# Optimization experiments

Measured on AMD Instinct MI355X. Metric: run time of the kernel, lower is better.

Reference implementation:

```python
import jax, jax.numpy as jnp
import numpy as np

NB_OBJECTS = 3
DIM_BODY = 10
DIM_OBJECT = 15
DIM_OBJ_FEAT = NB_OBJECTS + DIM_OBJECT  # 18
DIM_PHI_IN = 54
HID = 256
DIM_PHI_OUT = 256
DIM_RHO_OUT = 1
B = 65536

# (o1, o2) object pair and (j, k) predicate indices, as in the torch code
PAIRS = [((0, 1), (3, 5)), ((0, 2), (4, 7)), ((1, 2), (6, 8))]


def setup_inputs() -> dict:
    key = jax.random.key(0)
    ks = jax.random.split(key, 24)
    inp = {
        "obs": jax.random.normal(ks[0], (B, 55), dtype=jnp.float32),
        "ag": jax.random.uniform(ks[1], (B, 9), dtype=jnp.float32),
        "g": jax.random.uniform(ks[2], (B, 9), dtype=jnp.float32),
        "anchor_g": jax.random.uniform(ks[3], (B, 9), dtype=jnp.float32),
        "act": jax.random.normal(ks[4], (B, 4), dtype=jnp.float32),
    }
    s = 0.05
    # PhiCriticDeepSet: two independent 2-layer MLPs (streams 1 and 2)
    inp["w1"] = jax.random.normal(ks[5], (DIM_PHI_IN, HID), dtype=jnp.float32) * s
    inp["b1"] = jnp.zeros((HID,), dtype=jnp.float32)
    inp["w2"] = jax.random.normal(ks[6], (HID, DIM_PHI_OUT), dtype=jnp.float32) * s
    inp["b2"] = jnp.zeros((DIM_PHI_OUT,), dtype=jnp.float32)
    inp["w3"] = jax.random.normal(ks[7], (DIM_PHI_IN, HID), dtype=jnp.float32) * s
    inp["b3"] = jnp.zeros((HID,), dtype=jnp.float32)
    inp["w4"] = jax.random.normal(ks[8], (HID, DIM_PHI_OUT), dtype=jnp.float32) * s
    inp["b4"] = jnp.zeros((DIM_PHI_OUT,), dtype=jnp.float32)
    # RhoCriticDeepSet: two independent 2-layer heads
    inp["w5"] = jax.random.normal(ks[9], (DIM_PHI_OUT, HID), dtype=jnp.float32) * s
    inp["b5"] = jnp.zeros((HID,), dtype=jnp.float32)
    inp["w6"] = jax.random.normal(ks[10], (HID, DIM_RHO_OUT), dtype=jnp.float32) * s
    inp["b6"] = jnp.zeros((DIM_RHO_OUT,), dtype=jnp.float32)
    inp["w7"] = jax.random.normal(ks[11], (DIM_PHI_OUT, HID), dtype=jnp.float32) * s
    inp["b7"] = jnp.zeros((HID,), dtype=jnp.float32)
    inp["w8"] = jax.random.normal(ks[12], (HID, DIM_RHO_OUT), dtype=jnp.float32) * s
    inp["b8"] = jnp.zeros((DIM_RHO_OUT,), dtype=jnp.float32)
    return inp


def _build_pair_inputs(obs, ag, g, act, anchor_g):
    """combinations_trick branch: data-dependent gather of goal bits and object pairs."""
    bs = obs.shape[0]
    obs_body = obs[:, :DIM_BODY]
    eye = jnp.eye(NB_OBJECTS, dtype=obs.dtype)
    # obs_objects: [3, B, 18] = one-hot(3) ++ object state(15)
    obs_objects = jnp.stack([
        jnp.concatenate([jnp.broadcast_to(eye[i], (bs, NB_OBJECTS)),
                         obs[:, DIM_BODY + DIM_OBJECT * i: DIM_BODY + DIM_OBJECT * (i + 1)]],
                        axis=1)
        for i in range(NB_OBJECTS)], axis=0)
    bidx = jnp.arange(bs)
    inputs = []
    for i, ((o1, o2), (j, k)) in enumerate(PAIRS):
        # selector = anchor_g @ [e_j, e_k] difference = anchor_g[:, j] - anchor_g[:, k]
        sel = (anchor_g[:, j] - anchor_g[:, k]) >= 0  # [B] bool
        # idxs_bits[i] = [i, j] where sel else [i, k]
        bit2 = jnp.where(sel, j, k)  # [B] int
        ag_pair = jnp.stack([ag[:, i], ag[bidx, bit2]], axis=1)  # [B, 2]
        g_pair = jnp.stack([g[:, i], g[bidx, bit2]], axis=1)     # [B, 2]
        # idxs_objects[i] = [o1, o2] where sel else [o2, o1]
        oi = jnp.where(sel, o1, o2)  # [B]
        oj = jnp.where(sel, o2, o1)
        obj_first = obs_objects[oi, bidx]   # [B, 18] gather along object axis
        obj_second = obs_objects[oj, bidx]  # [B, 18]
        inputs.append(jnp.concatenate(
            [ag_pair, g_pair, obs_body, obj_first, obj_second, act], axis=1))
    return jnp.stack(inputs)  # [3, B, 54]


def reference(obs, ag, g, anchor_g, act,
              w1, b1, w2, b2, w3, b3, w4, b4,
              w5, b5, w6, b6, w7, b7, w8, b8):
    inp = _build_pair_inputs(obs, ag, g, act, anchor_g)  # [3, B, 54]
    # PhiCriticDeepSet (two relu-relu streams)
    x1 = jax.nn.relu(jnp.einsum('pbi,ih->pbh', jax.nn.relu(jnp.einsum('pbd,dh->pbh', inp, w1) + b1), w2) + b2)
    x2 = jax.nn.relu(jnp.einsum('pbi,ih->pbh', jax.nn.relu(jnp.einsum('pbd,dh->pbh', inp, w3) + b3), w4) + b4)
    s1 = x1.sum(axis=0)  # [B, 256] deepset sum over pairs
    s2 = x2.sum(axis=0)
    # RhoCriticDeepSet readouts
    q1 = jax.nn.relu(s1 @ w5 + b5) @ w6 + b6  # [B, 1]
    q2 = jax.nn.relu(s2 @ w7 + b7) @ w8 + b8  # [B, 1]
    return (q1, q2)
```

## Files before the change

### kernel.cpp

```cpp
#include <hip/hip_runtime.h>
#include <hip/hip_bf16.h>

typedef unsigned short u16;
typedef unsigned int   u32;

using bf8 = __attribute__((ext_vector_type(8))) __bf16;
using f4  = __attribute__((ext_vector_type(4))) float;

__device__ __forceinline__ float b2f(u16 u) {
    union { u32 i; float f; } v; v.i = ((u32)u) << 16; return v.f;
}
__device__ __forceinline__ u16 f2b(float f) {
    union { float f; u32 i; } v; v.f = f;
    u32 x = v.i;
    x += 0x7fffu + ((x >> 16) & 1u);
    return (u16)(x >> 16);
}
__device__ __forceinline__ u32 pk2(float lo, float hi) {
    union { __hip_bfloat162 h; u32 u; } v;
    v.h = __float22bfloat162_rn(make_float2(lo, hi));
    return v.u;
}

__global__ void swz_all(const float* __restrict__ w1, const float* __restrict__ w3,
                        const float* __restrict__ w2, const float* __restrict__ w4,
                        const float* __restrict__ w5, const float* __restrict__ w7,
                        u16* __restrict__ ws) {
    __shared__ u16 slab[32 * 270];
    int b = blockIdx.x, t = threadIdx.x;
    const float* src; u16* dst; int kmax, kt;
    if      (b <  2) { src = w1; dst = ws;          kmax = 54;  kt = b;      }
    else if (b <  4) { src = w3; dst = ws + 16384;  kmax = 54;  kt = b - 2;  }
    else if (b < 12) { src = w2; dst = ws + 32768;  kmax = 256; kt = b - 4;  }
    else if (b < 20) { src = w4; dst = ws + 98304;  kmax = 256; kt = b - 12; }
    else if (b < 28) { src = w5; dst = ws + 163840; kmax = 256; kt = b - 20; }
    else             { src = w7; dst = ws + 229376; kmax = 256; kt = b - 28; }

    #pragma unroll
    for (int it = 0; it < 8; ++it) {
        int flat = it * 1024 + t * 4;
        int row = flat >> 8, col = flat & 255;
        int k = kt * 32 + row;
        float4 v = make_float4(0.f, 0.f, 0.f, 0.f);
        if (k < kmax) v = *(const float4*)(src + k * 256 + col);
        u32* sp = (u32*)&slab[row * 270 + col];
        sp[0] = pk2(v.x, v.y);
        sp[1] = pk2(v.z, v.w);
    }
    __syncthreads();

    int lane = t & 63, wave = t >> 6, lr = lane & 15, kg = lane >> 4;
    #pragma unroll
    for (int i = 0; i < 4; ++i) {
        int ct = wave * 4 + i;
        u16 v[8];
        #pragma unroll
        for (int j = 0; j < 8; ++j)
            v[j] = slab[(kg * 8 + j) * 270 + ct * 16 + lr];
        uint4 o;
        o.x = (u32)v[0] | ((u32)v[1] << 16);
        o.y = (u32)v[2] | ((u32)v[3] << 16);
        o.z = (u32)v[4] | ((u32)v[5] << 16);
        o.w = (u32)v[6] | ((u32)v[7] << 16);
        *(uint4*)(dst + (size_t)(((kt * 16 + ct) * 64 + lane) * 8)) = o;
    }
}

#define H_OFF 6144
#define S2O   (32 * 256)
#define SBO   (H_OFF + 96 * 256)

__global__ __launch_bounds__(512) __attribute__((amdgpu_waves_per_eu(4, 4)))
void critic_kernel(
    const float* __restrict__ obs, const float* __restrict__ ag,
    const float* __restrict__ g,   const float* __restrict__ anchor,
    const float* __restrict__ act,
    const float* __restrict__ b1,  const float* __restrict__ b2,
    const float* __restrict__ b3,  const float* __restrict__ b4,
    const float* __restrict__ b5,  const float* __restrict__ b7,
    const float* __restrict__ w6,  const float* __restrict__ b6,
    const float* __restrict__ w8,  const float* __restrict__ b8,
    const u16* __restrict__ wsz, float* __restrict__ out, int B) {

    __shared__ u16 pool[SBO + 32 * 256];

    const int t    = threadIdx.x;
    const int lane = t & 63;
    const int wave = t >> 6;
    const int wr   = wave >> 2;
    const int wc   = wave & 3;
    const int lr   = lane & 15;
    const int lg   = lane >> 4;
    const int wg   = blockIdx.x;
    const int swr  = (lr & 7) << 3;

    if (t < 192) {
        const int O1[3] = {0, 0, 1}, O2[3] = {1, 2, 2};
        const int JA[3] = {3, 4, 6}, KA[3] = {5, 7, 8};
        int rr = t >> 1, part = t & 1;
        int p = rr >> 5, bl = rr & 31;
        int b = wg * 32 + bl;
        int j = JA[p], k = KA[p];
        bool sel = (anchor[b * 9 + j] - anchor[b * 9 + k]) >= 0.0f;
        u16* row = &pool[rr * 64];
        const int sw = (rr & 7) << 3;
        const u16 ONE = 0x3F80;
        if (part == 0) {
            int bit2 = sel ? j : k;
            int oi = sel ? O1[p] : O2[p];
            row[0 ^ sw] = f2b(ag[b * 9 + p]);
            row[1 ^ sw] = f2b(ag[b * 9 + bit2]);
            row[2 ^ sw] = f2b(g[b * 9 + p]);
            row[3 ^ sw] = f2b(g[b * 9 + bit2]);
            for (int c = 0; c < 10; ++c) row[(4 + c) ^ sw] = f2b(obs[b * 55 + c]);
            row[14 ^ sw] = (oi == 0) ? ONE : 0;
            row[15 ^ sw] = (oi == 1) ? ONE : 0;
            row[16 ^ sw] = (oi == 2) ? ONE : 0;
            for (int c = 0; c < 15; ++c) row[(17 + c) ^ sw] = f2b(obs[b * 55 + 10 + 15 * oi + c]);
        } else {
            int oj = sel ? O2[p] : O1[p];
            row[32 ^ sw] = (oj == 0) ? ONE : 0;
            row[33 ^ sw] = (oj == 1) ? ONE : 0;
            row[34 ^ sw] = (oj == 2) ? ONE : 0;
            for (int c = 0; c < 15; ++c) row[(35 + c) ^ sw] = f2b(obs[b * 55 + 10 + 15 * oj + c]);
            for (int c = 0; c < 4; ++c)  row[(50 + c) ^ sw] = f2b(act[b * 4 + c]);
            for (int c = 54; c < 64; ++c) row[c ^ sw] = 0;
        }
    }
    __syncthreads();

    u32 s2w[4][2];

    for (int net = 0; net < 2; ++net) {
        const u16* Wl1 = wsz + (net ? 16384 : 0);
        const u16* Wl2 = wsz + 32768 + (net ? 65536 : 0);
        const float* bl1 = net ? b3 : b1;
        const float* bl2 = net ? b4 : b2;

        f4 acc[3][4];
        #pragma unroll
        for (int p = 0; p < 3; ++p)
            #pragma unroll
            for (int c = 0; c < 4; ++c) acc[p][c] = (f4){0.f, 0.f, 0.f, 0.f};
        __builtin_amdgcn_s_setprio(1);
        #pragma unroll 1
        for (int kt = 0; kt < 2; ++kt) {
            bf8 wfr[4];
            #pragma unroll
            for (int c = 0; c < 4; ++c)
                wfr[c] = *(const bf8*)(Wl1 + (size_t)(((kt * 16 + wc * 4 + c) * 64 + lane) * 8));
            #pragma unroll
            for (int p = 0; p < 3; ++p) {
                bf8 xfr = *(const bf8*)(&pool[((2 * p + wr) * 16 + lr) * 64 + ((kt * 32 + lg * 8) ^ swr)]);
                #pragma unroll
                for (int c = 0; c < 4; ++c)
                    acc[p][c] = __builtin_amdgcn_mfma_f32_16x16x32_bf16(wfr[c], xfr, acc[p][c], 0, 0, 0);
            }
        }
        __builtin_amdgcn_s_setprio(0);
        #pragma unroll
        for (int c = 0; c < 4; ++c) {
            float4 bv = *(const float4*)(bl1 + (wc * 4 + c) * 16 + lg * 4);
            #pragma unroll
            for (int p = 0; p < 3; ++p) {
                uint2 w;
                w.x = pk2(fmaxf(acc[p][c][0] + bv.x, 0.f), fmaxf(acc[p][c][1] + bv.y, 0.f));
                w.y = pk2(fmaxf(acc[p][c][2] + bv.z, 0.f), fmaxf(acc[p][c][3] + bv.w, 0.f));
                *(uint2*)&pool[H_OFF + ((2 * p + wr) * 16 + lr) * 256 + ((((wc * 4 + c) * 16) + lg * 4) ^ swr)] = w;
            }
        }
        __syncthreads();

        f4 acc2[3][4];
        #pragma unroll
        for (int p = 0; p < 3; ++p)
            #pragma unroll
            for (int c = 0; c < 4; ++c) acc2[p][c] = (f4){0.f, 0.f, 0.f, 0.f};
        __builtin_amdgcn_s_setprio(1);
        #pragma unroll 1
        for (int ks = 0; ks < 8; ++ks) {
            bf8 wfr[4];
            #pragma unroll
            for (int c = 0; c < 4; ++c)
                wfr[c] = *(const bf8*)(Wl2 + (size_t)(((ks * 16 + wc * 4 + c) * 64 + lane) * 8));
            #pragma unroll
            for (int p = 0; p < 3; ++p) {
                bf8 hfr = *(const bf8*)(&pool[H_OFF + ((2 * p + wr) * 16 + lr) * 256 + ((ks * 32 + lg * 8) ^ swr)]);
                #pragma unroll
                for (int c = 0; c < 4; ++c)
                    acc2[p][c] = __builtin_amdgcn_mfma_f32_16x16x32_bf16(wfr[c], hfr, acc2[p][c], 0, 0, 0);
            }
        }
        __builtin_amdgcn_s_setprio(0);
        #pragma unroll
        for (int c = 0; c < 4; ++c) {
            float4 bv = *(const float4*)(bl2 + (wc * 4 + c) * 16 + lg * 4);
            f4 sv = (f4){0.f, 0.f, 0.f, 0.f};
            #pragma unroll
            for (int p = 0; p < 3; ++p) {
                sv[0] += fmaxf(acc2[p][c][0] + bv.x, 0.f);
                sv[1] += fmaxf(acc2[p][c][1] + bv.y, 0.f);
                sv[2] += fmaxf(acc2[p][c][2] + bv.z, 0.f);
                sv[3] += fmaxf(acc2[p][c][3] + bv.w, 0.f);
            }
            if (net == 0) {
                uint2 w;
                w.x = pk2(sv[0], sv[1]);
                w.y = pk2(sv[2], sv[3]);
                *(uint2*)&pool[SBO + (wr * 16 + lr) * 256 + ((((wc * 4 + c) * 16) + lg * 4) ^ swr)] = w;
            } else {
                s2w[c][0] = pk2(sv[0], sv[1]);
                s2w[c][1] = pk2(sv[2], sv[3]);
            }
        }
        __syncthreads();
    }

    #pragma unroll
    for (int c = 0; c < 4; ++c) {
        int base = H_OFF + S2O + (wr * 16 + lr) * 256 + ((((wc * 4 + c) * 16) + lg * 4) ^ swr);
        *(uint2*)&pool[base] = *(uint2*)&s2w[c][0];
    }
    __syncthreads();

    {
        const u16* Wr    = wsz + (wr ? 229376 : 163840);
        const int sbase  = wr ? (H_OFF + S2O) : SBO;
        const float* br  = wr ? b7 : b5;
        const float* wq  = wr ? w8 : w6;
        f4 racc[2][4];
        #pragma unroll
        for (int rt = 0; rt < 2; ++rt)
            #pragma unroll
            for (int c = 0; c < 4; ++c) racc[rt][c] = (f4){0.f, 0.f, 0.f, 0.f};
        __builtin_amdgcn_s_setprio(1);
        #pragma unroll 1
        for (int ks = 0; ks < 8; ++ks) {
            bf8 wf[4];
            #pragma unroll
            for (int c = 0; c < 4; ++c)
                wf[c] = *(const bf8*)(Wr + (size_t)(((ks * 16 + wc * 4 + c) * 64 + lane) * 8));
            #pragma unroll
            for (int rt = 0; rt < 2; ++rt) {
                bf8 sf = *(const bf8*)(&pool[sbase + (rt * 16 + lr) * 256 + ((ks * 32 + lg * 8) ^ swr)]);
                #pragma unroll
                for (int c = 0; c < 4; ++c)
                    racc[rt][c] = __builtin_amdgcn_mfma_f32_16x16x32_bf16(wf[c], sf, racc[rt][c], 0, 0, 0);
            }
        }
        __builtin_amdgcn_s_setprio(0);
        float part[2] = {0.f, 0.f};
        #pragma unroll
        for (int c = 0; c < 4; ++c) {
            float4 bv = *(const float4*)(br + (wc * 4 + c) * 16 + lg * 4);
            float4 wv = *(const float4*)(wq + (wc * 4 + c) * 16 + lg * 4);
            #pragma unroll
            for (int rt = 0; rt < 2; ++rt) {
                part[rt] += fmaxf(racc[rt][c][0] + bv.x, 0.f) * wv.x
                          + fmaxf(racc[rt][c][1] + bv.y, 0.f) * wv.y
                          + fmaxf(racc[rt][c][2] + bv.z, 0.f) * wv.z
                          + fmaxf(racc[rt][c][3] + bv.w, 0.f) * wv.w;
            }
        }
        #pragma unroll
        for (int rt = 0; rt < 2; ++rt) {
            part[rt] += __shfl_xor(part[rt], 16);
            part[rt] += __shfl_xor(part[rt], 32);
        }
        if (lane < 16) {
            float* fs = (float*)pool;
            fs[(wr * 32 + lane) * 4 + wc]      = part[0];
            fs[(wr * 32 + 16 + lane) * 4 + wc] = part[1];
        }
        __syncthreads();
    }

    if (t < 64) {
        int net = t >> 5, b = t & 31;
        const float* fs = (const float*)pool;
        float qv = net ? b8[0] : b6[0];
        #pragma unroll
        for (int p = 0; p < 4; ++p)
            qv += fs[(net * 32 + b) * 4 + p];
        out[net * B + wg * 32 + b] = qv;
    }
}

extern "C" void kernel_launch(void* const* d_in, const int* in_sizes, int n_in,
                              void* d_out, int out_size, void* d_ws, size_t ws_size,
                              hipStream_t stream) {
    const float* obs = (const float*)d_in[0];
    const float* ag  = (const float*)d_in[1];
    const float* g   = (const float*)d_in[2];
    const float* anc = (const float*)d_in[3];
    const float* act = (const float*)d_in[4];
    const float* w1  = (const float*)d_in[5];
    const float* b1  = (const float*)d_in[6];
    const float* w2  = (const float*)d_in[7];
    const float* b2  = (const float*)d_in[8];
    const float* w3  = (const float*)d_in[9];
    const float* b3  = (const float*)d_in[10];
    const float* w4  = (const float*)d_in[11];
    const float* b4  = (const float*)d_in[12];
    const float* w5  = (const float*)d_in[13];
    const float* b5  = (const float*)d_in[14];
    const float* w6  = (const float*)d_in[15];
    const float* b6  = (const float*)d_in[16];
    const float* w7  = (const float*)d_in[17];
    const float* b7  = (const float*)d_in[18];
    const float* w8  = (const float*)d_in[19];
    const float* b8  = (const float*)d_in[20];
    u16* ws    = (u16*)d_ws;
    float* out = (float*)d_out;
    int B = in_sizes[0] / 55;

    swz_all<<<36, 256, 0, stream>>>(w1, w3, w2, w4, w5, w7, ws);
    critic_kernel<<<(B + 31) / 32, 512, 0, stream>>>(obs, ag, g, anc, act,
                                                     b1, b2, b3, b4, b5, b7,
                                                     w6, b6, w8, b8, ws, out, B);
}
```

Baseline: 190.6 us.

## Halve batch tile to 16 rows with 4-wave blocks

Shrinks each block from 32 to 16 batch rows and from 8 to 4 waves. Waves now split only by output column, and the rho stage runs both heads in every wave instead of one head per wave-row. This halves shared memory per block and doubles the grid size, aiming for more resident blocks and better latency hiding. In exchange, every weight fragment loaded from global memory is reused across half as many rows, so weight traffic per sample doubles.

```diff
diff --git a/kernel.cpp b/kernel.cpp
--- a/kernel.cpp
+++ b/kernel.cpp
@@ -66,11 +66,11 @@
     }
 }
 
-#define H_OFF 6144
-#define S2O   (32 * 256)
-#define SBO   (H_OFF + 96 * 256)
-
-__global__ __launch_bounds__(512) __attribute__((amdgpu_waves_per_eu(4, 4)))
+#define H_OFF 3072
+#define S2O   (16 * 256)
+#define SBO   (H_OFF + 48 * 256)
+
+__global__ __launch_bounds__(256) __attribute__((amdgpu_waves_per_eu(4, 4)))
 void critic_kernel(
     const float* __restrict__ obs, const float* __restrict__ ag,
     const float* __restrict__ g,   const float* __restrict__ anchor,
@@ -82,24 +82,22 @@
     const float* __restrict__ w8,  const float* __restrict__ b8,
     const u16* __restrict__ wsz, float* __restrict__ out, int B) {
 
-    __shared__ u16 pool[SBO + 32 * 256];
+    __shared__ u16 pool[SBO + 16 * 256];
 
     const int t    = threadIdx.x;
     const int lane = t & 63;
-    const int wave = t >> 6;
-    const int wr   = wave >> 2;
-    const int wc   = wave & 3;
+    const int wc   = t >> 6;
     const int lr   = lane & 15;
     const int lg   = lane >> 4;
     const int wg   = blockIdx.x;
     const int swr  = (lr & 7) << 3;
 
-    if (t < 192) {
+    if (t < 96) {
         const int O1[3] = {0, 0, 1}, O2[3] = {1, 2, 2};
         const int JA[3] = {3, 4, 6}, KA[3] = {5, 7, 8};
         int rr = t >> 1, part = t & 1;
-        int p = rr >> 5, bl = rr & 31;
-        int b = wg * 32 + bl;
+        int p = rr >> 4, bl = rr & 15;
+        int b = wg * 16 + bl;
         int j = JA[p], k = KA[p];
         bool sel = (anchor[b * 9 + j] - anchor[b * 9 + k]) >= 0.0f;
         u16* row = &pool[rr * 64];
@@ -151,7 +149,7 @@
                 wfr[c] = *(const bf8*)(Wl1 + (size_t)(((kt * 16 + wc * 4 + c) * 64 + lane) * 8));
             #pragma unroll
             for (int p = 0; p < 3; ++p) {
-                bf8 xfr = *(const bf8*)(&pool[((2 * p + wr) * 16 + lr) * 64 + ((kt * 32 + lg * 8) ^ swr)]);
+                bf8 xfr = *(const bf8*)(&pool[(p * 16 + lr) * 64 + ((kt * 32 + lg * 8) ^ swr)]);
                 #pragma unroll
                 for (int c = 0; c < 4; ++c)
                     acc[p][c] = __builtin_amdgcn_mfma_f32_16x16x32_bf16(wfr[c], xfr, acc[p][c], 0, 0, 0);
@@ -166,7 +164,7 @@
                 uint2 w;
                 w.x = pk2(fmaxf(acc[p][c][0] + bv.x, 0.f), fmaxf(acc[p][c][1] + bv.y, 0.f));
                 w.y = pk2(fmaxf(acc[p][c][2] + bv.z, 0.f), fmaxf(acc[p][c][3] + bv.w, 0.f));
-                *(uint2*)&pool[H_OFF + ((2 * p + wr) * 16 + lr) * 256 + ((((wc * 4 + c) * 16) + lg * 4) ^ swr)] = w;
+                *(uint2*)&pool[H_OFF + (p * 16 + lr) * 256 + ((((wc * 4 + c) * 16) + lg * 4) ^ swr)] = w;
             }
         }
         __syncthreads();
@@ -185,7 +183,7 @@
                 wfr[c] = *(const bf8*)(Wl2 + (size_t)(((ks * 16 + wc * 4 + c) * 64 + lane) * 8));
             #pragma unroll
             for (int p = 0; p < 3; ++p) {
-                bf8 hfr = *(const bf8*)(&pool[H_OFF + ((2 * p + wr) * 16 + lr) * 256 + ((ks * 32 + lg * 8) ^ swr)]);
+                bf8 hfr = *(const bf8*)(&pool[H_OFF + (p * 16 + lr) * 256 + ((ks * 32 + lg * 8) ^ swr)]);
                 #pragma unroll
                 for (int c = 0; c < 4; ++c)
                     acc2[p][c] = __builtin_amdgcn_mfma_f32_16x16x32_bf16(wfr[c], hfr, acc2[p][c], 0, 0, 0);
@@ -207,7 +205,7 @@
                 uint2 w;
                 w.x = pk2(sv[0], sv[1]);
                 w.y = pk2(sv[2], sv[3]);
-                *(uint2*)&pool[SBO + (wr * 16 + lr) * 256 + ((((wc * 4 + c) * 16) + lg * 4) ^ swr)] = w;
+                *(uint2*)&pool[SBO + lr * 256 + ((((wc * 4 + c) * 16) + lg * 4) ^ swr)] = w;
             } else {
                 s2w[c][0] = pk2(sv[0], sv[1]);
                 s2w[c][1] = pk2(sv[2], sv[3]);
@@ -218,71 +216,73 @@
 
     #pragma unroll
     for (int c = 0; c < 4; ++c) {
-        int base = H_OFF + S2O + (wr * 16 + lr) * 256 + ((((wc * 4 + c) * 16) + lg * 4) ^ swr);
+        int base = H_OFF + S2O + lr * 256 + ((((wc * 4 + c) * 16) + lg * 4) ^ swr);
         *(uint2*)&pool[base] = *(uint2*)&s2w[c][0];
     }
     __syncthreads();
 
     {
-        const u16* Wr    = wsz + (wr ? 229376 : 163840);
-        const int sbase  = wr ? (H_OFF + S2O) : SBO;
-        const float* br  = wr ? b7 : b5;
-        const float* wq  = wr ? w8 : w6;
+        const u16* W5 = wsz + 163840;
+        const u16* W7 = wsz + 229376;
         f4 racc[2][4];
         #pragma unroll
-        for (int rt = 0; rt < 2; ++rt)
-            #pragma unroll
-            for (int c = 0; c < 4; ++c) racc[rt][c] = (f4){0.f, 0.f, 0.f, 0.f};
+        for (int ns = 0; ns < 2; ++ns)
+            #pragma unroll
+            for (int c = 0; c < 4; ++c) racc[ns][c] = (f4){0.f, 0.f, 0.f, 0.f};
         __builtin_amdgcn_s_setprio(1);
         #pragma unroll 1
         for (int ks = 0; ks < 8; ++ks) {
-            bf8 wf[4];
-            #pragma unroll
-            for (int c = 0; c < 4; ++c)
-                wf[c] = *(const bf8*)(Wr + (size_t)(((ks * 16 + wc * 4 + c) * 64 + lane) * 8));
-            #pragma unroll
-            for (int rt = 0; rt < 2; ++rt) {
-                bf8 sf = *(const bf8*)(&pool[sbase + (rt * 16 + lr) * 256 + ((ks * 32 + lg * 8) ^ swr)]);
+            #pragma unroll
+            for (int ns = 0; ns < 2; ++ns) {
+                const u16* Wr = ns ? W7 : W5;
+                const int sbase = ns ? (H_OFF + S2O) : SBO;
+                bf8 wf[4];
                 #pragma unroll
                 for (int c = 0; c < 4; ++c)
-                    racc[rt][c] = __builtin_amdgcn_mfma_f32_16x16x32_bf16(wf[c], sf, racc[rt][c], 0, 0, 0);
+                    wf[c] = *(const bf8*)(Wr + (size_t)(((ks * 16 + wc * 4 + c) * 64 + lane) * 8));
+                bf8 sf = *(const bf8*)(&pool[sbase + lr * 256 + ((ks * 32 + lg * 8) ^ swr)]);
+                #pragma unroll
+                for (int c = 0; c < 4; ++c)
+                    racc[ns][c] = __builtin_amdgcn_mfma_f32_16x16x32_bf16(wf[c], sf, racc[ns][c], 0, 0, 0);
             }
         }
         __builtin_amdgcn_s_setprio(0);
         float part[2] = {0.f, 0.f};
         #pragma unroll
-        for (int c = 0; c < 4; ++c) {
-            float4 bv = *(const float4*)(br + (wc * 4 + c) * 16 + lg * 4);
-            float4 wv = *(const float4*)(wq + (wc * 4 + c) * 16 + lg * 4);
-            #pragma unroll
-            for (int rt = 0; rt < 2; ++rt) {
-                part[rt] += fmaxf(racc[rt][c][0] + bv.x, 0.f) * wv.x
-                          + fmaxf(racc[rt][c][1] + bv.y, 0.f) * wv.y
-                          + fmaxf(racc[rt][c][2] + bv.z, 0.f) * wv.z
-                          + fmaxf(racc[rt][c][3] + bv.w, 0.f) * wv.w;
-            }
-        }
-        #pragma unroll
-        for (int rt = 0; rt < 2; ++rt) {
-            part[rt] += __shfl_xor(part[rt], 16);
-            part[rt] += __shfl_xor(part[rt], 32);
+        for (int ns = 0; ns < 2; ++ns) {
+            const float* br = ns ? b7 : b5;
+            const float* wq = ns ? w8 : w6;
+            #pragma unroll
+            for (int c = 0; c < 4; ++c) {
+                float4 bv = *(const float4*)(br + (wc * 4 + c) * 16 + lg * 4);
+                float4 wv = *(const float4*)(wq + (wc * 4 + c) * 16 + lg * 4);
+                part[ns] += fmaxf(racc[ns][c][0] + bv.x, 0.f) * wv.x
+                          + fmaxf(racc[ns][c][1] + bv.y, 0.f) * wv.y
+                          + fmaxf(racc[ns][c][2] + bv.z, 0.f) * wv.z
+                          + fmaxf(racc[ns][c][3] + bv.w, 0.f) * wv.w;
+            }
+        }
+        #pragma unroll
+        for (int ns = 0; ns < 2; ++ns) {
+            part[ns] += __shfl_xor(part[ns], 16);
+            part[ns] += __shfl_xor(part[ns], 32);
         }
         if (lane < 16) {
             float* fs = (float*)pool;
-            fs[(wr * 32 + lane) * 4 + wc]      = part[0];
-            fs[(wr * 32 + 16 + lane) * 4 + wc] = part[1];
+            fs[(0 * 16 + lane) * 4 + wc]  = part[0];
+            fs[(1 * 16 + lane) * 4 + wc]  = part[1];
         }
         __syncthreads();
     }
 
-    if (t < 64) {
-        int net = t >> 5, b = t & 31;
+    if (t < 32) {
+        int net = t >> 4, b = t & 15;
         const float* fs = (const float*)pool;
         float qv = net ? b8[0] : b6[0];
         #pragma unroll
         for (int p = 0; p < 4; ++p)
-            qv += fs[(net * 32 + b) * 4 + p];
-        out[net * B + wg * 32 + b] = qv;
+            qv += fs[(net * 16 + b) * 4 + p];
+        out[net * B + wg * 16 + b] = qv;
     }
 }
 
@@ -315,7 +315,7 @@
     int B = in_sizes[0] / 55;
 
     swz_all<<<36, 256, 0, stream>>>(w1, w3, w2, w4, w5, w7, ws);
-    critic_kernel<<<(B + 31) / 32, 512, 0, stream>>>(obs, ag, g, anc, act,
+    critic_kernel<<<(B + 15) / 16, 256, 0, stream>>>(obs, ag, g, anc, act,
                                                      b1, b2, b3, b4, b5, b7,
                                                      w6, b6, w8, b8, ws, out, B);
 }
```

New measurement: 208.9 us. 1.1x slower.
